# Optimization experiments

Hardware: AMD Instinct MI355X
Metric: run time of the kernel (lower is better)

The kernel has to match this reference:

```python
import jax, jax.numpy as jnp
import numpy as np

N_HEADS = 32
KV_HEADS = 8
HEAD_DIM = 128
D_MODEL = 4096
CLIP_QKV = 8.0
ROPE_THETA = 500000.0


def setup_inputs() -> dict:
    key = jax.random.key(0)
    k1, k2, k3 = jax.random.split(key, 3)
    x = jax.random.normal(k1, (2, 2048, D_MODEL), dtype=jnp.float32)
    Wqkv = jax.random.normal(k2, ((KV_HEADS * 2 + N_HEADS) * HEAD_DIM, D_MODEL), dtype=jnp.float32) * (D_MODEL ** -0.5)
    Wout = jax.random.normal(k3, (D_MODEL, D_MODEL), dtype=jnp.float32) * (D_MODEL ** -0.5)
    return {"x": x, "Wqkv": Wqkv, "Wout": Wout}


def _rope(t):
    # t: [B, H, L, D]; half-split (non-traditional) RoPE, offset=0
    B, H, L, D = t.shape
    half = D // 2
    inv_freq = 1.0 / (ROPE_THETA ** (jnp.arange(0, half, dtype=jnp.float32) / half))
    angles = jnp.arange(L, dtype=jnp.float32)[:, None] * inv_freq[None, :]  # [L, half]
    cos = jnp.cos(angles)[None, None]  # [1,1,L,half]
    sin = jnp.sin(angles)[None, None]
    t1, t2 = t[..., :half], t[..., half:]
    return jnp.concatenate([t1 * cos - t2 * sin, t2 * cos + t1 * sin], axis=-1).astype(t.dtype)


def reference(x, Wqkv, Wout):
    B, L, D = x.shape
    qkv = jnp.clip(x @ Wqkv.T, -CLIP_QKV, CLIP_QKV)
    q = qkv[..., :D_MODEL]
    k = qkv[..., D_MODEL:D_MODEL + KV_HEADS * HEAD_DIM]
    v = qkv[..., D_MODEL + KV_HEADS * HEAD_DIM:]
    q = q.reshape(B, L, N_HEADS, HEAD_DIM).transpose(0, 2, 1, 3)   # [B,H,L,d]
    k = k.reshape(B, L, KV_HEADS, HEAD_DIM).transpose(0, 2, 1, 3)  # [B,Hkv,L,d]
    v = v.reshape(B, L, KV_HEADS, HEAD_DIM).transpose(0, 2, 1, 3)
    q = _rope(q)
    k = _rope(k)
    # GQA: broadcast kv heads to query heads
    rep = N_HEADS // KV_HEADS
    k = jnp.repeat(k, rep, axis=1)  # [B,H,L,d]
    v = jnp.repeat(v, rep, axis=1)
    scale = HEAD_DIM ** -0.5
    scores = jnp.einsum('bhqd,bhkd->bhqk', q, k) * scale
    causal = jnp.tril(jnp.ones((L, L), dtype=bool))
    scores = jnp.where(causal[None, None], scores, jnp.finfo(scores.dtype).min)
    probs = jax.nn.softmax(scores, axis=-1)
    out = jnp.einsum('bhqk,bhkd->bhqd', probs, v)
    out = out.transpose(0, 2, 1, 3).reshape(B, L, D_MODEL)
    return out @ Wout.T
```

## Files before the change

kernel.cpp:

```cpp
#include <hip/hip_runtime.h>
#include <hip/hip_bf16.h>
#include <math.h>

typedef __hip_bfloat16 bf16;
typedef __attribute__((ext_vector_type(8))) short bf16x8;
typedef __attribute__((ext_vector_type(4))) short bf16x4;
typedef __attribute__((ext_vector_type(4))) float f32x4;

__device__ __forceinline__ void glds16(const bf16* g, bf16* l) {
    __builtin_amdgcn_global_load_lds(
        (const __attribute__((address_space(1))) void*)g,
        (__attribute__((address_space(3))) void*)l, 16, 0, 0);
}

__global__ __launch_bounds__(256)
void convert_to_bf16(const void* __restrict__ src, bf16* __restrict__ dst, long n) {
    const unsigned short* u16 = (const unsigned short*)src;
    int lane = threadIdx.x & 63;
    unsigned short u = u16[lane * 2];
    int e = (u >> 7) & 0xFF;
    int isf32 = __popcll(__ballot(e >= 0x86)) > 4;
    long i = ((long)blockIdx.x * 256 + threadIdx.x) * 8;
    if (i >= n) return;
    if (isf32) {
        const float* s = (const float*)src;
        bf16x8 o;
        #pragma unroll
        for (int j = 0; j < 8; j++) {
            bf16 b = (bf16)s[i + j];
            o[j] = *(short*)&b;
        }
        *(bf16x8*)(dst + i) = o;
    } else {
        *(bf16x8*)(dst + i) = *(const bf16x8*)((const bf16*)src + i);
    }
}

template<int BN, bool CLIP, typename OUT>
__global__ __launch_bounds__(512, 2)
void gemm256(const bf16* __restrict__ A, const bf16* __restrict__ B,
             OUT* __restrict__ C, int M, int N, int K) {
    constexpr int NB = BN / 64;
    constexpr int WN = BN / 4;
    __shared__ __align__(16) bf16 sA[2][256 * 64];
    __shared__ __align__(16) bf16 sB[2][BN * 64];

    const int tid   = threadIdx.x;
    const int lane  = tid & 63;
    const int row16 = lane & 15;
    const int quad  = lane >> 4;
    const int wid   = tid >> 6;
    const int wr    = wid >> 2;
    const int wc    = wid & 3;

    const int nwg  = gridDim.x * gridDim.y;
    const int orig = blockIdx.y * gridDim.x + blockIdx.x;
    const int cpx  = nwg >> 3;
    const int sw   = (orig & 7) * cpx + (orig >> 3);
    const int bn   = sw % gridDim.x;
    const int bm   = sw / gridDim.x;

    const int srow   = tid >> 3;
    const int schunk = (tid & 7) ^ (srow & 7);
    const bf16* gA = A + (size_t)(bm * 256) * K + schunk * 8;
    const bf16* gB = B + (size_t)(bn * BN) * K + schunk * 8;

    auto STAGE = [&](int u, int t) {
        #pragma unroll
        for (int q = 0; q < 4; q++)
            glds16(gA + (size_t)(q * 64 + srow) * K + t * 64,
                   &sA[u][0] + q * 4096 + tid * 8);
        #pragma unroll
        for (int q = 0; q < NB; q++)
            glds16(gB + (size_t)(q * 64 + srow) * K + t * 64,
                   &sB[u][0] + q * 4096 + tid * 8);
    };

    const int cx0 = ((quad) ^ (row16 & 7)) << 4;
    const int cx1 = ((4 + quad) ^ (row16 & 7)) << 4;
    const int aRowOff = (wr * 128 + row16) * 128;
    const int bRowOff = (wc * WN + row16) * 128;

    f32x4 acc[8][NB] = {};

    const int NT = K >> 6;
    STAGE(0, 0);
    STAGE(1, 1);
    if constexpr (NB == 4) asm volatile("s_waitcnt vmcnt(8)" ::: "memory");
    else                   asm volatile("s_waitcnt vmcnt(7)" ::: "memory");
    __builtin_amdgcn_sched_barrier(0);
    __builtin_amdgcn_s_barrier();

    for (int t = 0; t < NT; t++) {
        const int cur = t & 1;
        const char* aRd = (const char*)(&sA[cur][0]) + aRowOff;
        const char* bRd = (const char*)(&sB[cur][0]) + bRowOff;

        bf16x8 af0[8], bf0[NB], af1[8], bf1[NB];
        #pragma unroll
        for (int i = 0; i < 8; i++)
            af0[i] = *(const bf16x8*)(aRd + i * 2048 + cx0);
        #pragma unroll
        for (int j = 0; j < NB; j++)
            bf0[j] = *(const bf16x8*)(bRd + j * 2048 + cx0);
        __builtin_amdgcn_sched_barrier(0);
        #pragma unroll
        for (int i = 0; i < 8; i++)
            af1[i] = *(const bf16x8*)(aRd + i * 2048 + cx1);
        #pragma unroll
        for (int j = 0; j < NB; j++)
            bf1[j] = *(const bf16x8*)(bRd + j * 2048 + cx1);
        __builtin_amdgcn_sched_barrier(0);

        if constexpr (NB == 4) asm volatile("s_waitcnt lgkmcnt(12)" ::: "memory");
        else                   asm volatile("s_waitcnt lgkmcnt(11)" ::: "memory");
        __builtin_amdgcn_sched_barrier(0);

        __builtin_amdgcn_s_setprio(1);
        #pragma unroll
        for (int i = 0; i < 8; i++)
            #pragma unroll
            for (int j = 0; j < NB; j++)
                acc[i][j] = __builtin_amdgcn_mfma_f32_16x16x32_bf16(
                    af0[i], bf0[j], acc[i][j], 0, 0, 0);
        __builtin_amdgcn_s_setprio(0);
        __builtin_amdgcn_sched_barrier(0);

        asm volatile("s_waitcnt lgkmcnt(0)" ::: "memory");
        __builtin_amdgcn_sched_barrier(0);
        __builtin_amdgcn_s_barrier();

        if (t + 2 < NT) STAGE(cur, t + 2);
        __builtin_amdgcn_sched_barrier(0);

        __builtin_amdgcn_s_setprio(1);
        #pragma unroll
        for (int i = 0; i < 8; i++)
            #pragma unroll
            for (int j = 0; j < NB; j++)
                acc[i][j] = __builtin_amdgcn_mfma_f32_16x16x32_bf16(
                    af1[i], bf1[j], acc[i][j], 0, 0, 0);
        __builtin_amdgcn_s_setprio(0);
        __builtin_amdgcn_sched_barrier(0);

        if (t + 2 < NT) {
            if constexpr (NB == 4) asm volatile("s_waitcnt vmcnt(8)" ::: "memory");
            else                   asm volatile("s_waitcnt vmcnt(7)" ::: "memory");
        } else {
            asm volatile("s_waitcnt vmcnt(0)" ::: "memory");
        }
        __builtin_amdgcn_sched_barrier(0);
        __builtin_amdgcn_s_barrier();
    }

    #pragma unroll
    for (int i = 0; i < 8; i++) {
        #pragma unroll
        for (int j = 0; j < NB; j++) {
            #pragma unroll
            for (int v = 0; v < 4; v++) {
                float val = acc[i][j][v];
                if (CLIP) val = fminf(fmaxf(val, -8.0f), 8.0f);
                int grow = bm * 256 + wr * 128 + i * 16 + quad * 4 + v;
                int gcol = bn * BN + wc * WN + j * 16 + row16;
                C[(size_t)grow * N + gcol] = (OUT)val;
            }
        }
    }
}

__global__ __launch_bounds__(256)
void rope_reorder(const bf16* __restrict__ qkv, bf16* __restrict__ Q,
                  bf16* __restrict__ Kd, bf16* __restrict__ VT) {
    const int token = blockIdx.y;
    const int slot  = blockIdx.x * 4 + (threadIdx.x >> 6);
    const int lane  = threadIdx.x & 63;
    const int b = token >> 11, l = token & 2047;
    const bf16* src = qkv + (size_t)token * 6144 + slot * 128;
    if (slot < 40) {
        float x1 = __bfloat162float(src[lane]);
        float x2 = __bfloat162float(src[lane + 64]);
        float inv_freq = powf(500000.0f, -(float)lane * (1.0f / 64.0f));
        float ang = (float)l * inv_freq;
        float s, c;
        sincosf(ang, &s, &c);
        float o1 = x1 * c - x2 * s;
        float o2 = x2 * c + x1 * s;
        bf16* dst;
        if (slot < 32) dst = Q  + ((size_t)(b * 32 + slot)        * 2048 + l) * 128;
        else           dst = Kd + ((size_t)(b * 8  + (slot - 32)) * 2048 + l) * 128;
        dst[lane]      = (bf16)o1;
        dst[lane + 64] = (bf16)o2;
    } else {
        bf16* dst = VT + (size_t)(b * 8 + (slot - 40)) * 128 * 2048 + l;
        dst[(size_t)lane * 2048]        = src[lane];
        dst[(size_t)(lane + 64) * 2048] = src[lane + 64];
    }
}

#define SP_STR 72

__global__ __launch_bounds__(256, 3)
void attn_kernel(const bf16* __restrict__ Q, const bf16* __restrict__ K,
                 const bf16* __restrict__ V, bf16* __restrict__ Oout) {
    const int qt = 31 - blockIdx.x;
    const int bh = blockIdx.y;
    const int b = bh >> 5, h = bh & 31;
    const int kh = h >> 2;
    const bf16* Qp = Q + ((size_t)(b * 32 + h) * 2048 + qt * 64) * 128;
    const bf16* Kp = K + (size_t)(b * 8 + kh) * 2048 * 128;
    const bf16* Vp = V + (size_t)(b * 8 + kh) * 128 * 2048;

    __shared__ __align__(16) bf16 sK[64 * 128];
    __shared__ __align__(16) bf16 sV[128 * 64];
    __shared__ __align__(16) bf16 sP[4 * 16 * SP_STR];

    const int tid = threadIdx.x, lane = tid & 63, wave = tid >> 6;
    const int row = lane & 15, quad = lane >> 4;
    const int rx  = (row & 7) << 4;
    char* sKb = (char*)sK;
    char* sVb = (char*)sV;

    const int krow = tid >> 4;
    const int kc8  = (tid & 15) ^ (krow & 7);
    const int vrow = tid >> 3;
    const int vc8  = (tid & 7) ^ (vrow & 7);
    const int ldst = tid * 16;

    bf16x8 aq[4];
    #pragma unroll
    for (int kk = 0; kk < 4; kk++)
        aq[kk] = *(const bf16x8*)(Qp + (size_t)(wave * 16 + row) * 128 + (kk * 4 + quad) * 8);

    bf16x8 kpf[4], vpf[4];
    #pragma unroll
    for (int j = 0; j < 4; j++) {
        kpf[j] = *(const bf16x8*)(Kp + (size_t)(j * 16 + krow) * 128 + kc8 * 8);
        vpf[j] = *(const bf16x8*)(Vp + (size_t)(j * 32 + vrow) * 2048 + vc8 * 8);
    }
    #pragma unroll
    for (int j = 0; j < 4; j++) {
        *(bf16x8*)(sKb + ldst + j * 4096) = kpf[j];
        *(bf16x8*)(sVb + ldst + j * 4096) = vpf[j];
    }
    __syncthreads();

    float pm = -1e30f, pl = 0.0f;
    f32x4 o_acc[8] = {};
    const float scale = 0.08838834764831845f;

    for (int jj = 0; jj <= qt; jj++) {
        if (jj < qt) {
            #pragma unroll
            for (int j = 0; j < 4; j++) {
                kpf[j] = *(const bf16x8*)(Kp + (size_t)((jj + 1) * 64 + j * 16 + krow) * 128 + kc8 * 8);
                vpf[j] = *(const bf16x8*)(Vp + (size_t)(j * 32 + vrow) * 2048 + (jj + 1) * 64 + vc8 * 8);
            }
        }

        f32x4 s_acc[4] = {};
        __builtin_amdgcn_s_setprio(1);
        #pragma unroll
        for (int nt = 0; nt < 4; nt++) {
            #pragma unroll
            for (int kk = 0; kk < 4; kk++) {
                bf16x8 bk = *(const bf16x8*)(sKb + (nt * 16 + row) * 256
                                             + (((kk * 4 + quad) * 16) ^ rx));
                s_acc[nt] = __builtin_amdgcn_mfma_f32_16x16x32_bf16(
                    bk, aq[kk], s_acc[nt], 0, 0, 0);
            }
        }
        __builtin_amdgcn_s_setprio(0);

        #pragma unroll
        for (int nt = 0; nt < 4; nt++) {
            #pragma unroll
            for (int v = 0; v < 4; v++) {
                float s = s_acc[nt][v] * scale;
                if (jj == qt) {
                    int kpos = nt * 16 + quad * 4 + v;
                    int qrow = wave * 16 + row;
                    if (kpos > qrow) s = -1e30f;
                }
                s_acc[nt][v] = s;
            }
        }
        float m_loc = s_acc[0][0];
        #pragma unroll
        for (int nt = 0; nt < 4; nt++)
            #pragma unroll
            for (int v = 0; v < 4; v++)
                m_loc = fmaxf(m_loc, s_acc[nt][v]);
        m_loc = fmaxf(m_loc, __shfl_xor(m_loc, 16, 64));
        m_loc = fmaxf(m_loc, __shfl_xor(m_loc, 32, 64));

        if (!__all(m_loc - pm <= 8.0f)) {
            float mn = fmaxf(pm, m_loc);
            float al = __expf(pm - mn);
            pm = mn;
            pl *= al;
            float al_q[4];
            #pragma unroll
            for (int v = 0; v < 4; v++)
                al_q[v] = __shfl(al, quad * 4 + v, 64);
            #pragma unroll
            for (int dt = 0; dt < 8; dt++)
                #pragma unroll
                for (int v = 0; v < 4; v++)
                    o_acc[dt][v] *= al_q[v];
        }

        float rs = 0.0f;
        #pragma unroll
        for (int nt = 0; nt < 4; nt++) {
            bf16x4 pw;
            #pragma unroll
            for (int v = 0; v < 4; v++) {
                float p = __expf(s_acc[nt][v] - pm);
                rs += p;
                bf16 pb = (bf16)p;
                pw[v] = *(short*)&pb;
            }
            *(bf16x4*)(sP + (wave * 16 + row) * SP_STR + nt * 16 + quad * 4) = pw;
        }
        rs += __shfl_xor(rs, 16, 64);
        rs += __shfl_xor(rs, 32, 64);
        pl += rs;

        __builtin_amdgcn_s_setprio(1);
        #pragma unroll
        for (int kk = 0; kk < 2; kk++) {
            bf16x8 pa = *(const bf16x8*)(sP + (wave * 16 + row) * SP_STR + (kk * 4 + quad) * 8);
            #pragma unroll
            for (int dt = 0; dt < 8; dt++) {
                bf16x8 vb = *(const bf16x8*)(sVb + (dt * 16 + row) * 128
                                             + (((kk * 4 + quad) * 16) ^ rx));
                o_acc[dt] = __builtin_amdgcn_mfma_f32_16x16x32_bf16(
                    pa, vb, o_acc[dt], 0, 0, 0);
            }
        }
        __builtin_amdgcn_s_setprio(0);

        if (jj < qt) {
            __syncthreads();
            #pragma unroll
            for (int j = 0; j < 4; j++) {
                *(bf16x8*)(sKb + ldst + j * 4096) = kpf[j];
                *(bf16x8*)(sVb + ldst + j * 4096) = vpf[j];
            }
            __syncthreads();
        }
    }

    float pl_q[4];
    #pragma unroll
    for (int v = 0; v < 4; v++)
        pl_q[v] = __shfl(pl, quad * 4 + v, 64);
    const int token = b * 2048 + qt * 64 + wave * 16;
    #pragma unroll
    for (int dt = 0; dt < 8; dt++) {
        #pragma unroll
        for (int v = 0; v < 4; v++) {
            float o = o_acc[dt][v] / pl_q[v];
            int trow = token + quad * 4 + v;
            Oout[(size_t)trow * 4096 + h * 128 + dt * 16 + row] = (bf16)o;
        }
    }
}

extern "C" void kernel_launch(void* const* d_in, const int* in_sizes, int n_in,
                              void* d_out, int out_size, void* d_ws, size_t ws_size,
                              hipStream_t stream) {
    float* out = (float*)d_out;

    const size_t MB = 1024 * 1024;
    char* ws = (char*)d_ws;
    bf16* xb    = (bf16*)(ws);
    bf16* Wqkvb = (bf16*)(ws + 32 * MB);
    bf16* qkv   = (bf16*)(ws + 80 * MB);
    bf16* Qb    = (bf16*)(ws + 32 * MB);
    bf16* Kb    = (bf16*)(ws + 64 * MB);
    bf16* VTb   = (bf16*)(ws + 72 * MB);
    bf16* Woutb = (bf16*)(ws + 80 * MB);
    bf16* attn  = xb;

    convert_to_bf16<<<8192,  256, 0, stream>>>(d_in[0], xb,    16777216L);
    convert_to_bf16<<<12288, 256, 0, stream>>>(d_in[1], Wqkvb, 25165824L);
    gemm256<192, true, bf16><<<dim3(32, 16), 512, 0, stream>>>(xb, Wqkvb, qkv, 4096, 6144, 4096);
    rope_reorder<<<dim3(12, 4096), 256, 0, stream>>>(qkv, Qb, Kb, VTb);
    convert_to_bf16<<<8192,  256, 0, stream>>>(d_in[2], Woutb, 16777216L);
    attn_kernel<<<dim3(32, 64), 256, 0, stream>>>(Qb, Kb, VTb, attn);
    gemm256<256, false, float><<<dim3(16, 16), 512, 0, stream>>>(attn, Woutb, out, 4096, 4096, 4096);
}
```

Baseline: 788.6 us.

## Enlarge attention query tile to 128 rows with 8 waves sharing K/V tiles

The attention kernel now processes 128 query rows per block with 512 threads (8 waves), so each K/V tile loaded into shared memory serves twice as many query rows. Waves whose rows lie entirely before a key tile skip its compute, and the causal mask is applied only on diagonal tiles. The P scratch buffer switches from a padded stride to an XOR-swizzled layout, and the grid is reordered so heads vary fastest. This trades fewer blocks and more imbalance inside a block (idle waves on diagonal tiles) for lower K/V traffic and fewer loads per row.

Measured after the change: 979.8 us. 24.2% more time.

```diff
diff --git a/kernel.cpp b/kernel.cpp
--- a/kernel.cpp
+++ b/kernel.cpp
@@ -198,156 +198,162 @@
     }
 }
 
-#define SP_STR 72
-
-__global__ __launch_bounds__(256, 3)
+__global__ __launch_bounds__(512, 6)
 void attn_kernel(const bf16* __restrict__ Q, const bf16* __restrict__ K,
                  const bf16* __restrict__ V, bf16* __restrict__ Oout) {
-    const int qt = 31 - blockIdx.x;
-    const int bh = blockIdx.y;
+    const int qt = 15 - blockIdx.y;
+    const int bh = blockIdx.x;
     const int b = bh >> 5, h = bh & 31;
     const int kh = h >> 2;
-    const bf16* Qp = Q + ((size_t)(b * 32 + h) * 2048 + qt * 64) * 128;
+    const bf16* Qp = Q + ((size_t)(b * 32 + h) * 2048 + qt * 128) * 128;
     const bf16* Kp = K + (size_t)(b * 8 + kh) * 2048 * 128;
     const bf16* Vp = V + (size_t)(b * 8 + kh) * 128 * 2048;
 
     __shared__ __align__(16) bf16 sK[64 * 128];
     __shared__ __align__(16) bf16 sV[128 * 64];
-    __shared__ __align__(16) bf16 sP[4 * 16 * SP_STR];
+    __shared__ __align__(16) bf16 sP[8 * 16 * 64];
 
     const int tid = threadIdx.x, lane = tid & 63, wave = tid >> 6;
     const int row = lane & 15, quad = lane >> 4;
     const int rx  = (row & 7) << 4;
     char* sKb = (char*)sK;
     char* sVb = (char*)sV;
-
-    const int krow = tid >> 4;
-    const int kc8  = (tid & 15) ^ (krow & 7);
-    const int vrow = tid >> 3;
-    const int vc8  = (tid & 7) ^ (vrow & 7);
+    char* sPb = (char*)sP;
+
+    const int kr0 = tid >> 4;
+    const int kc8 = (tid & 15) ^ (kr0 & 7);
+    const int vr0 = tid >> 3;
+    const int vc8 = (tid & 7) ^ (vr0 & 7);
     const int ldst = tid * 16;
+    const bf16* kga = Kp + (size_t)kr0 * 128 + kc8 * 8;
+    const bf16* vga = Vp + (size_t)vr0 * 2048 + vc8 * 8;
 
     bf16x8 aq[4];
     #pragma unroll
     for (int kk = 0; kk < 4; kk++)
         aq[kk] = *(const bf16x8*)(Qp + (size_t)(wave * 16 + row) * 128 + (kk * 4 + quad) * 8);
 
-    bf16x8 kpf[4], vpf[4];
-    #pragma unroll
-    for (int j = 0; j < 4; j++) {
-        kpf[j] = *(const bf16x8*)(Kp + (size_t)(j * 16 + krow) * 128 + kc8 * 8);
-        vpf[j] = *(const bf16x8*)(Vp + (size_t)(j * 32 + vrow) * 2048 + vc8 * 8);
-    }
-    #pragma unroll
-    for (int j = 0; j < 4; j++) {
-        *(bf16x8*)(sKb + ldst + j * 4096) = kpf[j];
-        *(bf16x8*)(sVb + ldst + j * 4096) = vpf[j];
-    }
+    bf16x8 kpf[2], vpf[2];
+    kpf[0] = *(const bf16x8*)(kga);
+    kpf[1] = *(const bf16x8*)(kga + 4096);
+    vpf[0] = *(const bf16x8*)(vga);
+    vpf[1] = *(const bf16x8*)(vga + 131072);
+    *(bf16x8*)(sKb + ldst)        = kpf[0];
+    *(bf16x8*)(sKb + ldst + 8192) = kpf[1];
+    *(bf16x8*)(sVb + ldst)        = vpf[0];
+    *(bf16x8*)(sVb + ldst + 8192) = vpf[1];
     __syncthreads();
 
     float pm = -1e30f, pl = 0.0f;
     f32x4 o_acc[8] = {};
     const float scale = 0.08838834764831845f;
-
-    for (int jj = 0; jj <= qt; jj++) {
-        if (jj < qt) {
-            #pragma unroll
-            for (int j = 0; j < 4; j++) {
-                kpf[j] = *(const bf16x8*)(Kp + (size_t)((jj + 1) * 64 + j * 16 + krow) * 128 + kc8 * 8);
-                vpf[j] = *(const bf16x8*)(Vp + (size_t)(j * 32 + vrow) * 2048 + (jj + 1) * 64 + vc8 * 8);
-            }
-        }
-
-        f32x4 s_acc[4] = {};
-        __builtin_amdgcn_s_setprio(1);
-        #pragma unroll
-        for (int nt = 0; nt < 4; nt++) {
-            #pragma unroll
-            for (int kk = 0; kk < 4; kk++) {
-                bf16x8 bk = *(const bf16x8*)(sKb + (nt * 16 + row) * 256
+    const int NJ = 2 * qt + 2;
+    const int qrow_lane = qt * 128 + wave * 16 + row;
+    const int qrow_wmin = qt * 128 + wave * 16;
+    const int qrow_wmax = qrow_wmin + 15;
+
+    for (int jj = 0; jj < NJ; jj++) {
+        if (jj < NJ - 1) {
+            kpf[0] = *(const bf16x8*)(kga + (size_t)(jj + 1) * 8192);
+            kpf[1] = *(const bf16x8*)(kga + (size_t)(jj + 1) * 8192 + 4096);
+            vpf[0] = *(const bf16x8*)(vga + (jj + 1) * 64);
+            vpf[1] = *(const bf16x8*)(vga + (jj + 1) * 64 + 131072);
+        }
+
+        const bool active = (jj * 64 <= qrow_wmax);
+        if (active) {
+            f32x4 s_acc[4] = {};
+            __builtin_amdgcn_s_setprio(1);
+            #pragma unroll
+            for (int nt = 0; nt < 4; nt++) {
+                #pragma unroll
+                for (int kk = 0; kk < 4; kk++) {
+                    bf16x8 bk = *(const bf16x8*)(sKb + (nt * 16 + row) * 256
+                                                 + (((kk * 4 + quad) * 16) ^ rx));
+                    s_acc[nt] = __builtin_amdgcn_mfma_f32_16x16x32_bf16(
+                        bk, aq[kk], s_acc[nt], 0, 0, 0);
+                }
+            }
+            __builtin_amdgcn_s_setprio(0);
+
+            const bool needmask = (jj * 64 + 63 > qrow_wmin);
+            #pragma unroll
+            for (int nt = 0; nt < 4; nt++) {
+                #pragma unroll
+                for (int v = 0; v < 4; v++) {
+                    float s = s_acc[nt][v] * scale;
+                    if (needmask) {
+                        int kpos = jj * 64 + nt * 16 + quad * 4 + v;
+                        if (kpos > qrow_lane) s = -1e30f;
+                    }
+                    s_acc[nt][v] = s;
+                }
+            }
+            float m_loc = s_acc[0][0];
+            #pragma unroll
+            for (int nt = 0; nt < 4; nt++)
+                #pragma unroll
+                for (int v = 0; v < 4; v++)
+                    m_loc = fmaxf(m_loc, s_acc[nt][v]);
+            m_loc = fmaxf(m_loc, __shfl_xor(m_loc, 16, 64));
+            m_loc = fmaxf(m_loc, __shfl_xor(m_loc, 32, 64));
+
+            if (!__all(m_loc - pm <= 8.0f)) {
+                float mn = fmaxf(pm, m_loc);
+                float al = __expf(pm - mn);
+                pm = mn;
+                pl *= al;
+                float al_q[4];
+                #pragma unroll
+                for (int v = 0; v < 4; v++)
+                    al_q[v] = __shfl(al, quad * 4 + v, 64);
+                #pragma unroll
+                for (int dt = 0; dt < 8; dt++)
+                    #pragma unroll
+                    for (int v = 0; v < 4; v++)
+                        o_acc[dt][v] *= al_q[v];
+            }
+
+            float rs = 0.0f;
+            #pragma unroll
+            for (int nt = 0; nt < 4; nt++) {
+                bf16x4 pw;
+                #pragma unroll
+                for (int v = 0; v < 4; v++) {
+                    float p = __expf(s_acc[nt][v] - pm);
+                    rs += p;
+                    bf16 pb = (bf16)p;
+                    pw[v] = *(short*)&pb;
+                }
+                int slot = (2 * nt + (quad >> 1)) ^ (row & 7);
+                *(bf16x4*)(sPb + (wave * 16 + row) * 128 + slot * 16 + (quad & 1) * 8) = pw;
+            }
+            rs += __shfl_xor(rs, 16, 64);
+            rs += __shfl_xor(rs, 32, 64);
+            pl += rs;
+
+            __builtin_amdgcn_s_setprio(1);
+            #pragma unroll
+            for (int kk = 0; kk < 2; kk++) {
+                bf16x8 pa = *(const bf16x8*)(sPb + (wave * 16 + row) * 128
                                              + (((kk * 4 + quad) * 16) ^ rx));
-                s_acc[nt] = __builtin_amdgcn_mfma_f32_16x16x32_bf16(
-                    bk, aq[kk], s_acc[nt], 0, 0, 0);
-            }
-        }
-        __builtin_amdgcn_s_setprio(0);
-
-        #pragma unroll
-        for (int nt = 0; nt < 4; nt++) {
-            #pragma unroll
-            for (int v = 0; v < 4; v++) {
-                float s = s_acc[nt][v] * scale;
-                if (jj == qt) {
-                    int kpos = nt * 16 + quad * 4 + v;
-                    int qrow = wave * 16 + row;
-                    if (kpos > qrow) s = -1e30f;
+                #pragma unroll
+                for (int dt = 0; dt < 8; dt++) {
+                    bf16x8 vb = *(const bf16x8*)(sVb + (dt * 16 + row) * 128
+                                                 + (((kk * 4 + quad) * 16) ^ rx));
+                    o_acc[dt] = __builtin_amdgcn_mfma_f32_16x16x32_bf16(
+                        pa, vb, o_acc[dt], 0, 0, 0);
                 }
-                s_acc[nt][v] = s;
-            }
-        }
-        float m_loc = s_acc[0][0];
-        #pragma unroll
-        for (int nt = 0; nt < 4; nt++)
-            #pragma unroll
-            for (int v = 0; v < 4; v++)
-                m_loc = fmaxf(m_loc, s_acc[nt][v]);
-        m_loc = fmaxf(m_loc, __shfl_xor(m_loc, 16, 64));
-        m_loc = fmaxf(m_loc, __shfl_xor(m_loc, 32, 64));
-
-        if (!__all(m_loc - pm <= 8.0f)) {
-            float mn = fmaxf(pm, m_loc);
-            float al = __expf(pm - mn);
-            pm = mn;
-            pl *= al;
-            float al_q[4];
-            #pragma unroll
-            for (int v = 0; v < 4; v++)
-                al_q[v] = __shfl(al, quad * 4 + v, 64);
-            #pragma unroll
-            for (int dt = 0; dt < 8; dt++)
-                #pragma unroll
-                for (int v = 0; v < 4; v++)
-                    o_acc[dt][v] *= al_q[v];
-        }
-
-        float rs = 0.0f;
-        #pragma unroll
-        for (int nt = 0; nt < 4; nt++) {
-            bf16x4 pw;
-            #pragma unroll
-            for (int v = 0; v < 4; v++) {
-                float p = __expf(s_acc[nt][v] - pm);
-                rs += p;
-                bf16 pb = (bf16)p;
-                pw[v] = *(short*)&pb;
-            }
-            *(bf16x4*)(sP + (wave * 16 + row) * SP_STR + nt * 16 + quad * 4) = pw;
-        }
-        rs += __shfl_xor(rs, 16, 64);
-        rs += __shfl_xor(rs, 32, 64);
-        pl += rs;
-
-        __builtin_amdgcn_s_setprio(1);
-        #pragma unroll
-        for (int kk = 0; kk < 2; kk++) {
-            bf16x8 pa = *(const bf16x8*)(sP + (wave * 16 + row) * SP_STR + (kk * 4 + quad) * 8);
-            #pragma unroll
-            for (int dt = 0; dt < 8; dt++) {
-                bf16x8 vb = *(const bf16x8*)(sVb + (dt * 16 + row) * 128
-                                             + (((kk * 4 + quad) * 16) ^ rx));
-                o_acc[dt] = __builtin_amdgcn_mfma_f32_16x16x32_bf16(
-                    pa, vb, o_acc[dt], 0, 0, 0);
-            }
-        }
-        __builtin_amdgcn_s_setprio(0);
-
-        if (jj < qt) {
+            }
+            __builtin_amdgcn_s_setprio(0);
+        }
+
+        if (jj < NJ - 1) {
             __syncthreads();
-            #pragma unroll
-            for (int j = 0; j < 4; j++) {
-                *(bf16x8*)(sKb + ldst + j * 4096) = kpf[j];
-                *(bf16x8*)(sVb + ldst + j * 4096) = vpf[j];
-            }
+            *(bf16x8*)(sKb + ldst)        = kpf[0];
+            *(bf16x8*)(sKb + ldst + 8192) = kpf[1];
+            *(bf16x8*)(sVb + ldst)        = vpf[0];
+            *(bf16x8*)(sVb + ldst + 8192) = vpf[1];
             __syncthreads();
         }
     }
@@ -356,7 +362,7 @@
     #pragma unroll
     for (int v = 0; v < 4; v++)
         pl_q[v] = __shfl(pl, quad * 4 + v, 64);
-    const int token = b * 2048 + qt * 64 + wave * 16;
+    const int token = b * 2048 + qt * 128 + wave * 16;
     #pragma unroll
     for (int dt = 0; dt < 8; dt++) {
         #pragma unroll
@@ -389,6 +395,6 @@
     gemm256<192, true, bf16><<<dim3(32, 16), 512, 0, stream>>>(xb, Wqkvb, qkv, 4096, 6144, 4096);
     rope_reorder<<<dim3(12, 4096), 256, 0, stream>>>(qkv, Qb, Kb, VTb);
     convert_to_bf16<<<8192,  256, 0, stream>>>(d_in[2], Woutb, 16777216L);
-    attn_kernel<<<dim3(32, 64), 256, 0, stream>>>(Qb, Kb, VTb, attn);
+    attn_kernel<<<dim3(64, 16), 512, 0, stream>>>(Qb, Kb, VTb, attn);
     gemm256<256, false, float><<<dim3(16, 16), 512, 0, stream>>>(attn, Woutb, out, 4096, 4096, 4096);
 }
```
